# Kernel optimization log

Measured on AMD Instinct MI355X. Metric: run time of the kernel, lower is better.

The kernel has to match this reference:

```python
import jax, jax.numpy as jnp
import numpy as np

N, DM, H = 32, 256, 64  # n_features, d_model, d_model//4
EPS = 1e-5

def _ln(y, g, b):
    m = jnp.mean(y, axis=-1, keepdims=True)
    v = jnp.mean((y - m) ** 2, axis=-1, keepdims=True)
    return (y - m) * jax.lax.rsqrt(v + EPS) * g + b

def setup_inputs() -> dict:
    key = jax.random.key(0)
    ks = jax.random.split(key, 16)
    s = lambda *d: 1.0 / np.sqrt(d[-1])
    inp = {
        "x": jax.random.normal(ks[0], (16, 512, N), dtype=jnp.float32),
        # selection GRN (d_in=N, hidden=DM, d_out=N, skip=Identity)
        "g_fc1_w": jax.random.normal(ks[1], (DM, N)) * s(DM, N),
        "g_fc1_b": jnp.zeros((DM,)),
        "g_gate_w": jax.random.normal(ks[2], (N, DM)) * s(N, DM),
        "g_gate_b": jnp.zeros((N,)),
        "g_fc2_w": jax.random.normal(ks[3], (N, DM)) * s(N, DM),
        "g_fc2_b": jnp.zeros((N,)),
        "g_ln_g": jnp.ones((N,)),
        "g_ln_b": jnp.zeros((N,)),
        # per-feature GRNs stacked over N (d_in=1, hidden=H, d_out=DM)
        "f_fc1_w": jax.random.normal(ks[4], (N, H)),
        "f_fc1_b": jnp.zeros((N, H)),
        "f_gate_w": jax.random.normal(ks[5], (N, DM, H)) * s(N, DM, H),
        "f_gate_b": jnp.zeros((N, DM)),
        "f_fc2_w": jax.random.normal(ks[6], (N, DM, H)) * s(N, DM, H),
        "f_fc2_b": jnp.zeros((N, DM)),
        "f_skip_w": jax.random.normal(ks[7], (N, DM)),
        "f_skip_b": jnp.zeros((N, DM)),
        "f_ln_g": jnp.ones((N, DM)),
        "f_ln_b": jnp.zeros((N, DM)),
    }
    return inp

def reference(x, g_fc1_w, g_fc1_b, g_gate_w, g_gate_b, g_fc2_w, g_fc2_b, g_ln_g, g_ln_b,
              f_fc1_w, f_fc1_b, f_gate_w, f_gate_b, f_fc2_w, f_fc2_b, f_skip_w, f_skip_b,
              f_ln_g, f_ln_b):
    B, T, n = x.shape
    flat = x.reshape(B * T, n)  # [BT,N]
    # selection GRN (skip = identity since d_in == d_out)
    h = jax.nn.elu(flat @ g_fc1_w.T + g_fc1_b)            # [BT,DM]
    a = jax.nn.sigmoid(h @ g_gate_w.T + g_gate_b)         # [BT,N]
    h2 = h @ g_fc2_w.T + g_fc2_b                          # [BT,N]
    weights = jax.nn.softmax(_ln(a * h2 + flat, g_ln_g, g_ln_b), axis=-1)  # [BT,N]
    # per-feature GRNs, vectorized over N
    hf = jax.nn.elu(flat[:, :, None] * f_fc1_w + f_fc1_b)                 # [BT,N,H]
    af = jax.nn.sigmoid(jnp.einsum('bnh,ndh->bnd', hf, f_gate_w) + f_gate_b)  # [BT,N,DM]
    h2f = jnp.einsum('bnh,ndh->bnd', hf, f_fc2_w) + f_fc2_b               # [BT,N,DM]
    res = flat[:, :, None] * f_skip_w + f_skip_b                          # [BT,N,DM]
    proc = _ln(af * h2f + res, f_ln_g, f_ln_b)                            # [BT,N,DM]
    selected = jnp.einsum('bnd,bn->bd', proc, weights).reshape(B, T, -1)  # [B,T,DM]
    feat_weights = weights.reshape(B, T, n).mean(axis=1)                  # [B,N]
    return selected, feat_weights
```

## Files before the change

kernel.cpp:

```cpp
#include <hip/hip_runtime.h>
#include <math.h>

#define N   32
#define DM  256
#define H   64
#define BT  8192
#define T_SEQ 512

typedef __attribute__((ext_vector_type(8))) short bf16x8;
typedef __attribute__((ext_vector_type(4))) float f32x4;

__device__ __forceinline__ float elu_f(float v) {
    return fmaxf(v, __expf(fminf(v, 0.f)) - 1.f);
}
__device__ __forceinline__ float sigm_f(float v) {
    return 1.f / (1.f + __expf(-v));
}

__device__ __forceinline__ void split_pack8(const float* v, bf16x8& hi, bf16x8& lo) {
    unsigned u[8]; float lf[8];
#pragma unroll
    for (int i = 0; i < 8; i++) {
        u[i]  = __builtin_bit_cast(unsigned, v[i]);
        lf[i] = v[i] - __builtin_bit_cast(float, u[i] & 0xffff0000u);
    }
    unsigned hw[4], lw[4];
#pragma unroll
    for (int j = 0; j < 4; j++) {
        hw[j] = (u[2*j] >> 16) | (u[2*j+1] & 0xffff0000u);
        unsigned l0 = __builtin_bit_cast(unsigned, lf[2*j]);
        unsigned l1 = __builtin_bit_cast(unsigned, lf[2*j+1]);
        lw[j] = (l0 >> 16) | (l1 & 0xffff0000u);
    }
    uint4 h4 = make_uint4(hw[0], hw[1], hw[2], hw[3]);
    uint4 l4 = make_uint4(lw[0], lw[1], lw[2], lw[3]);
    hi = __builtin_bit_cast(bf16x8, h4);
    lo = __builtin_bit_cast(bf16x8, l4);
}

__global__ __launch_bounds__(256) void k_pack(const float* __restrict__ gw,
                                              const float* __restrict__ fw,
                                              short* __restrict__ bfrag) {
    int n = blockIdx.x >> 2, wc = blockIdx.x & 3;
    int wid = threadIdx.x >> 6, lane = threadIdx.x & 63;
    for (int it = wid; it < 16; it += 4) {
        int ks = it >> 3, ct = it & 7;
        const float* W = (ct < 4) ? gw : fw;
        int d  = wc * 64 + (ct & 3) * 16 + (lane & 15);
        int h0 = ks * 32 + (lane >> 4) * 8;
        const float* src = W + (n * DM + d) * H + h0;
        float v[8];
        float4 a = *(const float4*)src;
        float4 b = *(const float4*)(src + 4);
        v[0]=a.x; v[1]=a.y; v[2]=a.z; v[3]=a.w;
        v[4]=b.x; v[5]=b.y; v[6]=b.z; v[7]=b.w;
        bf16x8 hi, lo;
        split_pack8(v, hi, lo);
        short* dst = bfrag + (size_t)((((n*4 + wc)*2 + ks)*8 + ct)*2) * 512 + lane * 8;
        *(bf16x8*)dst         = hi;
        *(bf16x8*)(dst + 512) = lo;
    }
}

__global__ __launch_bounds__(256) void k_sel(const float* __restrict__ x,
                      const float* __restrict__ fc1w, const float* __restrict__ fc1b,
                      const float* __restrict__ gatew, const float* __restrict__ gateb,
                      const float* __restrict__ fc2w, const float* __restrict__ fc2b,
                      const float* __restrict__ lng, const float* __restrict__ lnb,
                      float* __restrict__ wsel, float* __restrict__ fwout) {
    int wid = threadIdx.x >> 6, lane = threadIdx.x & 63;
    int row = blockIdx.x * 4 + wid;
    int l31 = lane & 31;

    float xv = x[row * N + l31];

    int dm0 = lane * 4;
    float4 hb = *(const float4*)(fc1b + dm0);
    float h0 = hb.x, h1 = hb.y, h2 = hb.z, h3 = hb.w;
#pragma unroll
    for (int c4 = 0; c4 < 8; c4++) {
        float4 w0 = *(const float4*)(fc1w + (dm0 + 0) * N + c4 * 4);
        float4 w1 = *(const float4*)(fc1w + (dm0 + 1) * N + c4 * 4);
        float4 w2 = *(const float4*)(fc1w + (dm0 + 2) * N + c4 * 4);
        float4 w3 = *(const float4*)(fc1w + (dm0 + 3) * N + c4 * 4);
        float xb0 = __shfl(xv, c4 * 4 + 0);
        float xb1 = __shfl(xv, c4 * 4 + 1);
        float xb2 = __shfl(xv, c4 * 4 + 2);
        float xb3 = __shfl(xv, c4 * 4 + 3);
        h0 += w0.x * xb0 + w0.y * xb1 + w0.z * xb2 + w0.w * xb3;
        h1 += w1.x * xb0 + w1.y * xb1 + w1.z * xb2 + w1.w * xb3;
        h2 += w2.x * xb0 + w2.y * xb1 + w2.z * xb2 + w2.w * xb3;
        h3 += w3.x * xb0 + w3.y * xb1 + w3.z * xb2 + w3.w * xb3;
    }
    h0 = elu_f(h0); h1 = elu_f(h1); h2 = elu_f(h2); h3 = elu_f(h3);

    float av = 0.f, bv = 0.f;
#pragma unroll
    for (int nn = 0; nn < N; nn++) {
        float4 g = *(const float4*)(gatew + nn * DM + dm0);
        float4 f = *(const float4*)(fc2w  + nn * DM + dm0);
        float pa = g.x * h0 + g.y * h1 + g.z * h2 + g.w * h3;
        float pb = f.x * h0 + f.y * h1 + f.z * h2 + f.w * h3;
#pragma unroll
        for (int m = 1; m < 64; m <<= 1) {
            pa += __shfl_xor(pa, m);
            pb += __shfl_xor(pb, m);
        }
        if (l31 == nn) { av = pa; bv = pb; }
    }

    float a  = sigm_f(av + gateb[l31]);
    float b2 = bv + fc2b[l31];
    float y  = a * b2 + xv;

    float s1 = y, s2 = y * y;
#pragma unroll
    for (int m = 1; m < 32; m <<= 1) { s1 += __shfl_xor(s1, m); s2 += __shfl_xor(s2, m); }
    float mean = s1 * (1.f / 32.f);
    float var  = s2 * (1.f / 32.f) - mean * mean;
    float xn = (y - mean) * rsqrtf(var + 1e-5f) * lng[l31] + lnb[l31];
    float mx = xn;
#pragma unroll
    for (int m = 1; m < 32; m <<= 1) mx = fmaxf(mx, __shfl_xor(mx, m));
    float e = __expf(xn - mx);
    float es = e;
#pragma unroll
    for (int m = 1; m < 32; m <<= 1) es += __shfl_xor(es, m);
    float w = e / es;

    if (lane < 32) {
        wsel[row * N + l31] = w;
        atomicAdd(fwout + (row >> 9) * N + l31, w * (1.f / (float)T_SEQ));
    }
}

__global__ __launch_bounds__(256, 1) void k_feat(
        const float* __restrict__ x,
        const float* __restrict__ f1w, const float* __restrict__ f1b,
        const short* __restrict__ bfrag,
        const float* __restrict__ gb,  const float* __restrict__ fb,
        const float* __restrict__ skw, const float* __restrict__ skb,
        const float* __restrict__ lng, const float* __restrict__ lnb,
        const float* __restrict__ wsel, float* __restrict__ out) {
    __shared__ float  xs[32 * 33];
    __shared__ float  wss[32 * 33];
    __shared__ float2 part[4][32];
    __shared__ float2 stat[32];

    int t = threadIdx.x;
    int wc = t >> 6, lane = t & 63;
    int l15 = lane & 15, lg = lane >> 4;
    int R0 = blockIdx.x * 32;

#pragma unroll
    for (int i = 0; i < 4; i++) {
        int idx = i * 256 + t;
        int r = idx >> 5, c = idx & 31;
        xs[r * 33 + c]  = x[(R0 + r) * N + c];
        wss[r * 33 + c] = wsel[(R0 + r) * N + c];
    }
    __syncthreads();

    f32x4 sel[2][4];
#pragma unroll
    for (int rt = 0; rt < 2; rt++)
#pragma unroll
        for (int ct = 0; ct < 4; ct++) sel[rt][ct] = (f32x4)(0.f);

    const short* bwc = bfrag + (size_t)(wc * 2) * 8 * 2 * 512;

#pragma unroll 1
    for (int n = 0; n < N; n++) {
        int dbase = n * DM + wc * 64 + l15;
        float gbv[4], fbv[4], skwv[4], skbv[4], lngv[4], lnbv[4];
#pragma unroll
        for (int ct = 0; ct < 4; ct++) {
            gbv[ct]  = gb [dbase + ct * 16];
            fbv[ct]  = fb [dbase + ct * 16];
            skwv[ct] = skw[dbase + ct * 16];
            skbv[ct] = skb[dbase + ct * 16];
            lngv[ct] = lng[dbase + ct * 16];
            lnbv[ct] = lnb[dbase + ct * 16];
        }

        bf16x8 ahi[2][2], alo[2][2];
#pragma unroll
        for (int ks = 0; ks < 2; ks++) {
            int h0 = ks * 32 + lg * 8;
            float4 w0 = *(const float4*)(f1w + n * H + h0);
            float4 w1 = *(const float4*)(f1w + n * H + h0 + 4);
            float4 b0 = *(const float4*)(f1b + n * H + h0);
            float4 b1 = *(const float4*)(f1b + n * H + h0 + 4);
#pragma unroll
            for (int rt = 0; rt < 2; rt++) {
                float xa = xs[(rt * 16 + l15) * 33 + n];
                float v[8];
                v[0] = elu_f(xa * w0.x + b0.x);
                v[1] = elu_f(xa * w0.y + b0.y);
                v[2] = elu_f(xa * w0.z + b0.z);
                v[3] = elu_f(xa * w0.w + b0.w);
                v[4] = elu_f(xa * w1.x + b1.x);
                v[5] = elu_f(xa * w1.y + b1.y);
                v[6] = elu_f(xa * w1.z + b1.z);
                v[7] = elu_f(xa * w1.w + b1.w);
                split_pack8(v, ahi[ks][rt], alo[ks][rt]);
            }
        }

        f32x4 acc[2][8];
#pragma unroll
        for (int rt = 0; rt < 2; rt++)
#pragma unroll
            for (int ct = 0; ct < 8; ct++)
                acc[rt][ct] = (f32x4)(ct < 4 ? gbv[ct] : fbv[ct - 4]);

        const short* bn = bwc + (size_t)n * 4 * 2 * 8 * 2 * 512;
#pragma unroll
        for (int ks = 0; ks < 2; ks++) {
#pragma unroll
            for (int ct = 0; ct < 8; ct++) {
                const short* bp = bn + ((ks * 8 + ct) * 2) * 512 + lane * 8;
                bf16x8 bhi = *(const bf16x8*)bp;
                bf16x8 blo = *(const bf16x8*)(bp + 512);
#pragma unroll
                for (int rt = 0; rt < 2; rt++) {
                    acc[rt][ct] = __builtin_amdgcn_mfma_f32_16x16x32_bf16(ahi[ks][rt], bhi, acc[rt][ct], 0, 0, 0);
                    acc[rt][ct] = __builtin_amdgcn_mfma_f32_16x16x32_bf16(alo[ks][rt], bhi, acc[rt][ct], 0, 0, 0);
                    acc[rt][ct] = __builtin_amdgcn_mfma_f32_16x16x32_bf16(ahi[ks][rt], blo, acc[rt][ct], 0, 0, 0);
                }
            }
        }

#pragma unroll
        for (int rt = 0; rt < 2; rt++) {
#pragma unroll
            for (int r4 = 0; r4 < 4; r4++) {
                int rowl = rt * 16 + lg * 4 + r4;
                float xa = xs[rowl * 33 + n];
                float s1 = 0.f, s2 = 0.f;
#pragma unroll
                for (int ct = 0; ct < 4; ct++) {
                    float a  = sigm_f(acc[rt][ct][r4]);
                    float yy = a * acc[rt][ct + 4][r4] + xa * skwv[ct] + skbv[ct];
                    acc[rt][ct + 4][r4] = yy;
                    s1 += yy; s2 += yy * yy;
                }
#pragma unroll
                for (int m = 1; m < 16; m <<= 1) {
                    s1 += __shfl_xor(s1, m);
                    s2 += __shfl_xor(s2, m);
                }
                if (l15 == 0) part[wc][rowl] = make_float2(s1, s2);
            }
        }
        __syncthreads();
        if (t < 32) {
            float s1 = part[0][t].x + part[1][t].x + part[2][t].x + part[3][t].x;
            float s2 = part[0][t].y + part[1][t].y + part[2][t].y + part[3][t].y;
            float mean = s1 * (1.f / (float)DM);
            float var  = s2 * (1.f / (float)DM) - mean * mean;
            stat[t] = make_float2(mean, rsqrtf(var + 1e-5f));
        }
        __syncthreads();

#pragma unroll
        for (int rt = 0; rt < 2; rt++) {
#pragma unroll
            for (int r4 = 0; r4 < 4; r4++) {
                int rowl = rt * 16 + lg * 4 + r4;
                float2 st = stat[rowl];
                float wv = wss[rowl * 33 + n];
#pragma unroll
                for (int ct = 0; ct < 4; ct++) {
                    float proc = (acc[rt][ct + 4][r4] - st.x) * st.y * lngv[ct] + lnbv[ct];
                    sel[rt][ct][r4] += proc * wv;
                }
            }
        }
    }

#pragma unroll
    for (int rt = 0; rt < 2; rt++)
#pragma unroll
        for (int r4 = 0; r4 < 4; r4++) {
            int row = R0 + rt * 16 + lg * 4 + r4;
#pragma unroll
            for (int ct = 0; ct < 4; ct++)
                out[row * DM + wc * 64 + ct * 16 + l15] = sel[rt][ct][r4];
        }
}

extern "C" void kernel_launch(void* const* d_in, const int* in_sizes, int n_in,
                              void* d_out, int out_size, void* d_ws, size_t ws_size,
                              hipStream_t stream) {
    const float* x        = (const float*)d_in[0];
    const float* g_fc1_w  = (const float*)d_in[1];
    const float* g_fc1_b  = (const float*)d_in[2];
    const float* g_gate_w = (const float*)d_in[3];
    const float* g_gate_b = (const float*)d_in[4];
    const float* g_fc2_w  = (const float*)d_in[5];
    const float* g_fc2_b  = (const float*)d_in[6];
    const float* g_ln_g   = (const float*)d_in[7];
    const float* g_ln_b   = (const float*)d_in[8];
    const float* f_fc1_w  = (const float*)d_in[9];
    const float* f_fc1_b  = (const float*)d_in[10];
    const float* f_gate_w = (const float*)d_in[11];
    const float* f_gate_b = (const float*)d_in[12];
    const float* f_fc2_w  = (const float*)d_in[13];
    const float* f_fc2_b  = (const float*)d_in[14];
    const float* f_skip_w = (const float*)d_in[15];
    const float* f_skip_b = (const float*)d_in[16];
    const float* f_ln_g   = (const float*)d_in[17];
    const float* f_ln_b   = (const float*)d_in[18];

    float* out_sel = (float*)d_out;
    float* out_fw  = (float*)d_out + BT * DM;

    float* ws_w  = (float*)d_ws;
    short* bfrag = (short*)((float*)d_ws + BT * N);

    hipMemsetAsync(out_fw, 0, 16 * N * sizeof(float), stream);

    k_pack<<<N * 4, 256, 0, stream>>>(f_gate_w, f_fc2_w, bfrag);

    k_sel<<<BT / 4, 256, 0, stream>>>(x, g_fc1_w, g_fc1_b, g_gate_w, g_gate_b,
                                      g_fc2_w, g_fc2_b, g_ln_g, g_ln_b,
                                      ws_w, out_fw);

    k_feat<<<BT / 32, 256, 0, stream>>>(x, f_fc1_w, f_fc1_b, bfrag,
                                        f_gate_b, f_fc2_b,
                                        f_skip_w, f_skip_b, f_ln_g, f_ln_b,
                                        ws_w, out_sel);
}
```

Baseline: 393.6 us.

## Rebalance work: smaller feature tiles, 4 rows per wave in selection, separate mean kernel

The feature-GRN kernel now handles 16 rows per block instead of 32, which gives 512 blocks and allows 2 blocks per CU. It replaces the two-barrier stats reduction with a double-buffered partial-sum array and a single barrier per feature. The selection kernel processes 4 rows per wave so weight loads are reused across rows, and the atomic feature-weight mean is replaced by a dedicated reduction kernel, which also removes the memset. The pack kernel's grid is widened to use more blocks. Each weight fragment is now loaded once per 16 rows instead of 32, which doubles B-fragment traffic per row in exchange for better occupancy.

Measured after the change: 342.0 us. -13.1%, faster.

```diff
diff --git a/kernel.cpp b/kernel.cpp
--- a/kernel.cpp
+++ b/kernel.cpp
@@ -41,10 +41,10 @@
 __global__ __launch_bounds__(256) void k_pack(const float* __restrict__ gw,
                                               const float* __restrict__ fw,
                                               short* __restrict__ bfrag) {
-    int n = blockIdx.x >> 2, wc = blockIdx.x & 3;
+    int blk = blockIdx.x;
+    int ks = blk & 1, wc = (blk >> 1) & 3, n = blk >> 3;
     int wid = threadIdx.x >> 6, lane = threadIdx.x & 63;
-    for (int it = wid; it < 16; it += 4) {
-        int ks = it >> 3, ct = it & 7;
+    for (int ct = wid; ct < 8; ct += 4) {
         const float* W = (ct < 4) ? gw : fw;
         int d  = wc * 64 + (ct & 3) * 16 + (lane & 15);
         int h0 = ks * 32 + (lane >> 4) * 8;
@@ -67,74 +67,107 @@
                       const float* __restrict__ gatew, const float* __restrict__ gateb,
                       const float* __restrict__ fc2w, const float* __restrict__ fc2b,
                       const float* __restrict__ lng, const float* __restrict__ lnb,
-                      float* __restrict__ wsel, float* __restrict__ fwout) {
+                      float* __restrict__ wsel) {
     int wid = threadIdx.x >> 6, lane = threadIdx.x & 63;
-    int row = blockIdx.x * 4 + wid;
     int l31 = lane & 31;
-
-    float xv = x[row * N + l31];
+    int row0 = blockIdx.x * 16 + wid * 4;
+
+    float xv[4];
+#pragma unroll
+    for (int r = 0; r < 4; r++) xv[r] = x[(row0 + r) * N + l31];
 
     int dm0 = lane * 4;
     float4 hb = *(const float4*)(fc1b + dm0);
-    float h0 = hb.x, h1 = hb.y, h2 = hb.z, h3 = hb.w;
+    float h[4][4];
+#pragma unroll
+    for (int r = 0; r < 4; r++) { h[r][0]=hb.x; h[r][1]=hb.y; h[r][2]=hb.z; h[r][3]=hb.w; }
 #pragma unroll
     for (int c4 = 0; c4 < 8; c4++) {
         float4 w0 = *(const float4*)(fc1w + (dm0 + 0) * N + c4 * 4);
         float4 w1 = *(const float4*)(fc1w + (dm0 + 1) * N + c4 * 4);
         float4 w2 = *(const float4*)(fc1w + (dm0 + 2) * N + c4 * 4);
         float4 w3 = *(const float4*)(fc1w + (dm0 + 3) * N + c4 * 4);
-        float xb0 = __shfl(xv, c4 * 4 + 0);
-        float xb1 = __shfl(xv, c4 * 4 + 1);
-        float xb2 = __shfl(xv, c4 * 4 + 2);
-        float xb3 = __shfl(xv, c4 * 4 + 3);
-        h0 += w0.x * xb0 + w0.y * xb1 + w0.z * xb2 + w0.w * xb3;
-        h1 += w1.x * xb0 + w1.y * xb1 + w1.z * xb2 + w1.w * xb3;
-        h2 += w2.x * xb0 + w2.y * xb1 + w2.z * xb2 + w2.w * xb3;
-        h3 += w3.x * xb0 + w3.y * xb1 + w3.z * xb2 + w3.w * xb3;
-    }
-    h0 = elu_f(h0); h1 = elu_f(h1); h2 = elu_f(h2); h3 = elu_f(h3);
-
-    float av = 0.f, bv = 0.f;
+#pragma unroll
+        for (int r = 0; r < 4; r++) {
+            float xb0 = __shfl(xv[r], c4 * 4 + 0);
+            float xb1 = __shfl(xv[r], c4 * 4 + 1);
+            float xb2 = __shfl(xv[r], c4 * 4 + 2);
+            float xb3 = __shfl(xv[r], c4 * 4 + 3);
+            h[r][0] += w0.x * xb0 + w0.y * xb1 + w0.z * xb2 + w0.w * xb3;
+            h[r][1] += w1.x * xb0 + w1.y * xb1 + w1.z * xb2 + w1.w * xb3;
+            h[r][2] += w2.x * xb0 + w2.y * xb1 + w2.z * xb2 + w2.w * xb3;
+            h[r][3] += w3.x * xb0 + w3.y * xb1 + w3.z * xb2 + w3.w * xb3;
+        }
+    }
+#pragma unroll
+    for (int r = 0; r < 4; r++)
+#pragma unroll
+        for (int j = 0; j < 4; j++) h[r][j] = elu_f(h[r][j]);
+
+    float av[4], bv[4];
 #pragma unroll
     for (int nn = 0; nn < N; nn++) {
         float4 g = *(const float4*)(gatew + nn * DM + dm0);
         float4 f = *(const float4*)(fc2w  + nn * DM + dm0);
-        float pa = g.x * h0 + g.y * h1 + g.z * h2 + g.w * h3;
-        float pb = f.x * h0 + f.y * h1 + f.z * h2 + f.w * h3;
-#pragma unroll
-        for (int m = 1; m < 64; m <<= 1) {
-            pa += __shfl_xor(pa, m);
-            pb += __shfl_xor(pb, m);
-        }
-        if (l31 == nn) { av = pa; bv = pb; }
-    }
-
-    float a  = sigm_f(av + gateb[l31]);
-    float b2 = bv + fc2b[l31];
-    float y  = a * b2 + xv;
-
-    float s1 = y, s2 = y * y;
-#pragma unroll
-    for (int m = 1; m < 32; m <<= 1) { s1 += __shfl_xor(s1, m); s2 += __shfl_xor(s2, m); }
-    float mean = s1 * (1.f / 32.f);
-    float var  = s2 * (1.f / 32.f) - mean * mean;
-    float xn = (y - mean) * rsqrtf(var + 1e-5f) * lng[l31] + lnb[l31];
-    float mx = xn;
-#pragma unroll
-    for (int m = 1; m < 32; m <<= 1) mx = fmaxf(mx, __shfl_xor(mx, m));
-    float e = __expf(xn - mx);
-    float es = e;
-#pragma unroll
-    for (int m = 1; m < 32; m <<= 1) es += __shfl_xor(es, m);
-    float w = e / es;
-
-    if (lane < 32) {
-        wsel[row * N + l31] = w;
-        atomicAdd(fwout + (row >> 9) * N + l31, w * (1.f / (float)T_SEQ));
-    }
-}
-
-__global__ __launch_bounds__(256, 1) void k_feat(
+#pragma unroll
+        for (int r = 0; r < 4; r++) {
+            float pa = g.x * h[r][0] + g.y * h[r][1] + g.z * h[r][2] + g.w * h[r][3];
+            float pb = f.x * h[r][0] + f.y * h[r][1] + f.z * h[r][2] + f.w * h[r][3];
+#pragma unroll
+            for (int m = 1; m < 64; m <<= 1) {
+                pa += __shfl_xor(pa, m);
+                pb += __shfl_xor(pb, m);
+            }
+            if (l31 == nn) { av[r] = pa; bv[r] = pb; }
+        }
+    }
+
+    float gb_ = gateb[l31], fb_ = fc2b[l31], lgv = lng[l31], lbv = lnb[l31];
+#pragma unroll
+    for (int r = 0; r < 4; r++) {
+        float a  = sigm_f(av[r] + gb_);
+        float b2 = bv[r] + fb_;
+        float y  = a * b2 + xv[r];
+        float s1 = y, s2 = y * y;
+#pragma unroll
+        for (int m = 1; m < 32; m <<= 1) { s1 += __shfl_xor(s1, m); s2 += __shfl_xor(s2, m); }
+        float mean = s1 * (1.f / 32.f);
+        float var  = s2 * (1.f / 32.f) - mean * mean;
+        float xn = (y - mean) * rsqrtf(var + 1e-5f) * lgv + lbv;
+        float mx = xn;
+#pragma unroll
+        for (int m = 1; m < 32; m <<= 1) mx = fmaxf(mx, __shfl_xor(mx, m));
+        float e = __expf(xn - mx);
+        float es = e;
+#pragma unroll
+        for (int m = 1; m < 32; m <<= 1) es += __shfl_xor(es, m);
+        float w = e / es;
+        if (lane < 32) wsel[(row0 + r) * N + l31] = w;
+    }
+}
+
+__global__ __launch_bounds__(256) void k_fw(const float* __restrict__ wsel,
+                                            float* __restrict__ fwout) {
+    __shared__ float part[8][32];
+    int b = blockIdx.x, t = threadIdx.x;
+    int n = t & 31, rg = t >> 5;
+    float s = 0.f;
+#pragma unroll 8
+    for (int j = 0; j < 64; j++) {
+        int r = rg + j * 8;
+        s += wsel[(b * T_SEQ + r) * N + n];
+    }
+    part[rg][n] = s;
+    __syncthreads();
+    if (t < 32) {
+        float tot = 0.f;
+#pragma unroll
+        for (int i = 0; i < 8; i++) tot += part[i][t];
+        fwout[b * N + t] = tot * (1.f / (float)T_SEQ);
+    }
+}
+
+__global__ __launch_bounds__(256, 2) void k_feat(
         const float* __restrict__ x,
         const float* __restrict__ f1w, const float* __restrict__ f1b,
         const short* __restrict__ bfrag,
@@ -142,18 +175,17 @@
         const float* __restrict__ skw, const float* __restrict__ skb,
         const float* __restrict__ lng, const float* __restrict__ lnb,
         const float* __restrict__ wsel, float* __restrict__ out) {
-    __shared__ float  xs[32 * 33];
-    __shared__ float  wss[32 * 33];
-    __shared__ float2 part[4][32];
-    __shared__ float2 stat[32];
+    __shared__ float  xs[16 * 33];
+    __shared__ float  wss[16 * 33];
+    __shared__ float2 part[2][4][16];
 
     int t = threadIdx.x;
     int wc = t >> 6, lane = t & 63;
     int l15 = lane & 15, lg = lane >> 4;
-    int R0 = blockIdx.x * 32;
-
-#pragma unroll
-    for (int i = 0; i < 4; i++) {
+    int R0 = blockIdx.x * 16;
+
+#pragma unroll
+    for (int i = 0; i < 2; i++) {
         int idx = i * 256 + t;
         int r = idx >> 5, c = idx & 31;
         xs[r * 33 + c]  = x[(R0 + r) * N + c];
@@ -161,11 +193,9 @@
     }
     __syncthreads();
 
-    f32x4 sel[2][4];
-#pragma unroll
-    for (int rt = 0; rt < 2; rt++)
-#pragma unroll
-        for (int ct = 0; ct < 4; ct++) sel[rt][ct] = (f32x4)(0.f);
+    f32x4 sel[4];
+#pragma unroll
+    for (int ct = 0; ct < 4; ct++) sel[ct] = (f32x4)(0.f);
 
     const short* bwc = bfrag + (size_t)(wc * 2) * 8 * 2 * 512;
 
@@ -183,7 +213,7 @@
             lnbv[ct] = lnb[dbase + ct * 16];
         }
 
-        bf16x8 ahi[2][2], alo[2][2];
+        bf16x8 ahi[2], alo[2];
 #pragma unroll
         for (int ks = 0; ks < 2; ks++) {
             int h0 = ks * 32 + lg * 8;
@@ -191,28 +221,23 @@
             float4 w1 = *(const float4*)(f1w + n * H + h0 + 4);
             float4 b0 = *(const float4*)(f1b + n * H + h0);
             float4 b1 = *(const float4*)(f1b + n * H + h0 + 4);
-#pragma unroll
-            for (int rt = 0; rt < 2; rt++) {
-                float xa = xs[(rt * 16 + l15) * 33 + n];
-                float v[8];
-                v[0] = elu_f(xa * w0.x + b0.x);
-                v[1] = elu_f(xa * w0.y + b0.y);
-                v[2] = elu_f(xa * w0.z + b0.z);
-                v[3] = elu_f(xa * w0.w + b0.w);
-                v[4] = elu_f(xa * w1.x + b1.x);
-                v[5] = elu_f(xa * w1.y + b1.y);
-                v[6] = elu_f(xa * w1.z + b1.z);
-                v[7] = elu_f(xa * w1.w + b1.w);
-                split_pack8(v, ahi[ks][rt], alo[ks][rt]);
-            }
-        }
-
-        f32x4 acc[2][8];
-#pragma unroll
-        for (int rt = 0; rt < 2; rt++)
-#pragma unroll
-            for (int ct = 0; ct < 8; ct++)
-                acc[rt][ct] = (f32x4)(ct < 4 ? gbv[ct] : fbv[ct - 4]);
+            float xa = xs[l15 * 33 + n];
+            float v[8];
+            v[0] = elu_f(xa * w0.x + b0.x);
+            v[1] = elu_f(xa * w0.y + b0.y);
+            v[2] = elu_f(xa * w0.z + b0.z);
+            v[3] = elu_f(xa * w0.w + b0.w);
+            v[4] = elu_f(xa * w1.x + b1.x);
+            v[5] = elu_f(xa * w1.y + b1.y);
+            v[6] = elu_f(xa * w1.z + b1.z);
+            v[7] = elu_f(xa * w1.w + b1.w);
+            split_pack8(v, ahi[ks], alo[ks]);
+        }
+
+        f32x4 acc[8];
+#pragma unroll
+        for (int ct = 0; ct < 8; ct++)
+            acc[ct] = (f32x4)(ct < 4 ? gbv[ct] : fbv[ct - 4]);
 
         const short* bn = bwc + (size_t)n * 4 * 2 * 8 * 2 * 512;
 #pragma unroll
@@ -222,72 +247,60 @@
                 const short* bp = bn + ((ks * 8 + ct) * 2) * 512 + lane * 8;
                 bf16x8 bhi = *(const bf16x8*)bp;
                 bf16x8 blo = *(const bf16x8*)(bp + 512);
-#pragma unroll
-                for (int rt = 0; rt < 2; rt++) {
-                    acc[rt][ct] = __builtin_amdgcn_mfma_f32_16x16x32_bf16(ahi[ks][rt], bhi, acc[rt][ct], 0, 0, 0);
-                    acc[rt][ct] = __builtin_amdgcn_mfma_f32_16x16x32_bf16(alo[ks][rt], bhi, acc[rt][ct], 0, 0, 0);
-                    acc[rt][ct] = __builtin_amdgcn_mfma_f32_16x16x32_bf16(ahi[ks][rt], blo, acc[rt][ct], 0, 0, 0);
-                }
-            }
-        }
-
-#pragma unroll
-        for (int rt = 0; rt < 2; rt++) {
-#pragma unroll
-            for (int r4 = 0; r4 < 4; r4++) {
-                int rowl = rt * 16 + lg * 4 + r4;
-                float xa = xs[rowl * 33 + n];
-                float s1 = 0.f, s2 = 0.f;
-#pragma unroll
-                for (int ct = 0; ct < 4; ct++) {
-                    float a  = sigm_f(acc[rt][ct][r4]);
-                    float yy = a * acc[rt][ct + 4][r4] + xa * skwv[ct] + skbv[ct];
-                    acc[rt][ct + 4][r4] = yy;
-                    s1 += yy; s2 += yy * yy;
-                }
-#pragma unroll
-                for (int m = 1; m < 16; m <<= 1) {
-                    s1 += __shfl_xor(s1, m);
-                    s2 += __shfl_xor(s2, m);
-                }
-                if (l15 == 0) part[wc][rowl] = make_float2(s1, s2);
-            }
+                acc[ct] = __builtin_amdgcn_mfma_f32_16x16x32_bf16(ahi[ks], bhi, acc[ct], 0, 0, 0);
+                acc[ct] = __builtin_amdgcn_mfma_f32_16x16x32_bf16(alo[ks], bhi, acc[ct], 0, 0, 0);
+                acc[ct] = __builtin_amdgcn_mfma_f32_16x16x32_bf16(ahi[ks], blo, acc[ct], 0, 0, 0);
+            }
+        }
+
+        int buf = n & 1;
+#pragma unroll
+        for (int r4 = 0; r4 < 4; r4++) {
+            int rowl = lg * 4 + r4;
+            float xa = xs[rowl * 33 + n];
+            float s1 = 0.f, s2 = 0.f;
+#pragma unroll
+            for (int ct = 0; ct < 4; ct++) {
+                float a  = sigm_f(acc[ct][r4]);
+                float yy = a * acc[ct + 4][r4] + xa * skwv[ct] + skbv[ct];
+                acc[ct + 4][r4] = yy;
+                s1 += yy; s2 += yy * yy;
+            }
+#pragma unroll
+            for (int m = 1; m < 16; m <<= 1) {
+                s1 += __shfl_xor(s1, m);
+                s2 += __shfl_xor(s2, m);
+            }
+            if (l15 == 0) part[buf][wc][rowl] = make_float2(s1, s2);
         }
         __syncthreads();
-        if (t < 32) {
-            float s1 = part[0][t].x + part[1][t].x + part[2][t].x + part[3][t].x;
-            float s2 = part[0][t].y + part[1][t].y + part[2][t].y + part[3][t].y;
+
+#pragma unroll
+        for (int r4 = 0; r4 < 4; r4++) {
+            int rowl = lg * 4 + r4;
+            float s1 = part[buf][0][rowl].x + part[buf][1][rowl].x
+                     + part[buf][2][rowl].x + part[buf][3][rowl].x;
+            float s2 = part[buf][0][rowl].y + part[buf][1][rowl].y
+                     + part[buf][2][rowl].y + part[buf][3][rowl].y;
             float mean = s1 * (1.f / (float)DM);
             float var  = s2 * (1.f / (float)DM) - mean * mean;
-            stat[t] = make_float2(mean, rsqrtf(var + 1e-5f));
-        }
-        __syncthreads();
-
-#pragma unroll
-        for (int rt = 0; rt < 2; rt++) {
-#pragma unroll
-            for (int r4 = 0; r4 < 4; r4++) {
-                int rowl = rt * 16 + lg * 4 + r4;
-                float2 st = stat[rowl];
-                float wv = wss[rowl * 33 + n];
-#pragma unroll
-                for (int ct = 0; ct < 4; ct++) {
-                    float proc = (acc[rt][ct + 4][r4] - st.x) * st.y * lngv[ct] + lnbv[ct];
-                    sel[rt][ct][r4] += proc * wv;
-                }
-            }
-        }
-    }
-
-#pragma unroll
-    for (int rt = 0; rt < 2; rt++)
-#pragma unroll
-        for (int r4 = 0; r4 < 4; r4++) {
-            int row = R0 + rt * 16 + lg * 4 + r4;
-#pragma unroll
-            for (int ct = 0; ct < 4; ct++)
-                out[row * DM + wc * 64 + ct * 16 + l15] = sel[rt][ct][r4];
-        }
+            float rs = rsqrtf(var + 1e-5f);
+            float wv = wss[rowl * 33 + n];
+#pragma unroll
+            for (int ct = 0; ct < 4; ct++) {
+                float proc = (acc[ct + 4][r4] - mean) * rs * lngv[ct] + lnbv[ct];
+                sel[ct][r4] += proc * wv;
+            }
+        }
+    }
+
+#pragma unroll
+    for (int r4 = 0; r4 < 4; r4++) {
+        int row = R0 + lg * 4 + r4;
+#pragma unroll
+        for (int ct = 0; ct < 4; ct++)
+            out[row * DM + wc * 64 + ct * 16 + l15] = sel[ct][r4];
+    }
 }
 
 extern "C" void kernel_launch(void* const* d_in, const int* in_sizes, int n_in,
@@ -319,15 +332,15 @@
     float* ws_w  = (float*)d_ws;
     short* bfrag = (short*)((float*)d_ws + BT * N);
 
-    hipMemsetAsync(out_fw, 0, 16 * N * sizeof(float), stream);
-
-    k_pack<<<N * 4, 256, 0, stream>>>(f_gate_w, f_fc2_w, bfrag);
-
-    k_sel<<<BT / 4, 256, 0, stream>>>(x, g_fc1_w, g_fc1_b, g_gate_w, g_gate_b,
-                                      g_fc2_w, g_fc2_b, g_ln_g, g_ln_b,
-                                      ws_w, out_fw);
-
-    k_feat<<<BT / 32, 256, 0, stream>>>(x, f_fc1_w, f_fc1_b, bfrag,
+    k_pack<<<256, 256, 0, stream>>>(f_gate_w, f_fc2_w, bfrag);
+
+    k_sel<<<BT / 16, 256, 0, stream>>>(x, g_fc1_w, g_fc1_b, g_gate_w, g_gate_b,
+                                       g_fc2_w, g_fc2_b, g_ln_g, g_ln_b,
+                                       ws_w);
+
+    k_fw<<<16, 256, 0, stream>>>(ws_w, out_fw);
+
+    k_feat<<<BT / 16, 256, 0, stream>>>(x, f_fc1_w, f_fc1_b, bfrag,
                                         f_gate_b, f_fc2_b,
                                         f_skip_w, f_skip_b, f_ln_g, f_ln_b,
                                         ws_w, out_sel);
```
